# Performance work log

Measured on AMD Instinct MI355X. Metric: run time of the kernel, lower is better.

Reference implementation:

```python
import jax, jax.numpy as jnp
import numpy as np

N, E, H, NF, EF = 50000, 400000, 128, 10, 10


def setup_inputs() -> dict:
    key = jax.random.key(0)
    ks = iter(jax.random.split(key, 24))
    rn = lambda shape, s=0.1: jax.random.normal(next(ks), shape, jnp.float32) * s
    z = lambda shape: jnp.zeros(shape, jnp.float32)
    o = lambda shape: jnp.ones(shape, jnp.float32)
    return {
        "x": jax.random.normal(next(ks), (N, NF), jnp.float32),
        "edge_index": jax.random.randint(next(ks), (2, E), 0, N, jnp.int32),
        "edge_attr": jax.random.normal(next(ks), (E, EF), jnp.float32),
        "ne_w": rn((NF, H)), "ne_b": z(H), "ne_g": o(H), "ne_beta": z(H),
        "ee_w": rn((EF, H)), "ee_b": z(H), "ee_g": o(H), "ee_beta": z(H),
        "gate_w": rn((3 * H, H)), "gate_b": z(H),
        "gatA_w": rn((2, H, H)), "gatA_asrc": rn((2, 8, 16)), "gatA_adst": rn((2, 8, 16)), "gatA_bias": z((2, H)),
        "gatB_w": rn((H, H)), "gatB_asrc": rn((1, H)), "gatB_adst": rn((1, H)), "gatB_bias": z(H),
        "ln_g": o((3, H)), "ln_b": z((3, H)),
        "c1_w": rn((2 * H, H)), "c1_b": z(H), "cl1_g": o(H), "cl1_b": z(H),
        "c2_w": rn((H, H // 2)), "c2_b": z(H // 2), "cl2_g": o(H // 2), "cl2_b": z(H // 2),
        "c3_w": rn((H // 2, 2)), "c3_b": z(2),
    }


def _ln(x, g, b):
    m = x.mean(-1, keepdims=True)
    v = ((x - m) ** 2).mean(-1, keepdims=True)
    return (x - m) / jnp.sqrt(v + 1e-5) * g + b


def _gat(h, src, dst, n, w, asrc, adst, bias, concat):
    # PyG GATConv: lin (no bias), per-edge leaky_relu score, segment softmax over dst, scatter-add
    heads, dout = asrc.shape
    xp = (h @ w).reshape(n, heads, dout)             # [N, heads, dout]
    a_s = (xp * asrc).sum(-1)                        # [N, heads]
    a_d = (xp * adst).sum(-1)
    e = jax.nn.leaky_relu(a_s[src] + a_d[dst], 0.2)  # [E2, heads]
    m = jax.ops.segment_max(e, dst, num_segments=n)
    ex = jnp.exp(e - m[dst])
    s = jax.ops.segment_sum(ex, dst, num_segments=n)
    alpha = ex / s[dst]                               # [E2, heads]
    out = jax.ops.segment_sum(xp[src] * alpha[..., None], dst, num_segments=n)  # [N, heads, dout]
    out = out.reshape(n, heads * dout) if concat else out.mean(1)
    return out + bias


def reference(x, edge_index, edge_attr, ne_w, ne_b, ne_g, ne_beta, ee_w, ee_b, ee_g, ee_beta,
              gate_w, gate_b, gatA_w, gatA_asrc, gatA_adst, gatA_bias, gatB_w, gatB_asrc,
              gatB_adst, gatB_bias, ln_g, ln_b, c1_w, c1_b, cl1_g, cl1_b, c2_w, c2_b,
              cl2_g, cl2_b, c3_w, c3_b):
    n = x.shape[0]
    row, col = edge_index[0], edge_index[1]
    loops = jnp.arange(n, dtype=edge_index.dtype)     # GATConv add_self_loops=True
    src_sl = jnp.concatenate([row, loops])
    dst_sl = jnp.concatenate([col, loops])

    h = jax.nn.relu(_ln(x @ ne_w + ne_b, ne_g, ne_beta))      # node encoder (dropout=eval)
    for l in range(2):
        h = _gat(h, src_sl, dst_sl, n, gatA_w[l], gatA_asrc[l], gatA_adst[l], gatA_bias[l], True)
        h = jax.nn.relu(_ln(h, ln_g[l], ln_b[l]))
    h = _gat(h, src_sl, dst_sl, n, gatB_w, gatB_asrc, gatB_adst, gatB_bias, False)
    h = jax.nn.relu(_ln(h, ln_g[2], ln_b[2]))

    s = h[row]
    d = h[col]
    e = jax.nn.relu(_ln(edge_attr @ ee_w + ee_b, ee_g, ee_beta))  # edge encoder
    gate = jax.nn.sigmoid(jnp.concatenate([s, d, e], axis=1) @ gate_w + gate_b)
    s = s + gate * e
    d = d + gate * e

    zc = jax.nn.relu(_ln(jnp.concatenate([s, d], axis=1) @ c1_w + c1_b, cl1_g, cl1_b))
    zc = jax.nn.relu(_ln(zc @ c2_w + c2_b, cl2_g, cl2_b))
    return zc @ c3_w + c3_b                                   # [E, num_classes]
```

## Files before the change

### kernel.cpp

```cpp
#include <hip/hip_runtime.h>
#include <hip/hip_bf16.h>

#define H 128
#define NFEAT 10
#define EFEAT 10
#define XPS 144

typedef __attribute__((ext_vector_type(8))) short bf16x8;
typedef __attribute__((ext_vector_type(4))) float f32x4;
typedef __attribute__((ext_vector_type(16))) float f32x16;
typedef __attribute__((ext_vector_type(4))) unsigned u32x4;
typedef __attribute__((ext_vector_type(2))) unsigned u32x2;

__device__ __forceinline__ float bflo(unsigned v) { return __uint_as_float(v << 16); }
__device__ __forceinline__ float bfhi(unsigned v) { return __uint_as_float(v & 0xffff0000u); }
__device__ __forceinline__ unsigned bfpack(float a, float b) {
    __hip_bfloat16 h0 = __float2bfloat16(a), h1 = __float2bfloat16(b);
    return (unsigned)(*(unsigned short*)&h0) | ((unsigned)(*(unsigned short*)&h1) << 16);
}
__device__ __forceinline__ bf16x8 cast8(u32x4 v) { return __builtin_bit_cast(bf16x8, v); }

__device__ __forceinline__ bf16x8 frag_from_pack(const unsigned* w, int b2) {
    u32x4 t;
    t.x = w[b2 * 4 + 0];
    t.y = w[b2 * 4 + 1];
    t.z = w[b2 * 4 + 2];
    t.w = w[b2 * 4 + 3];
    return cast8(t);
}

template<int NT>
__device__ __forceinline__ void bias_ln_relu_pack(f32x16* acc, const float* __restrict__ bias,
        const float* __restrict__ g, const float* __restrict__ beta,
        int hh, float invn, unsigned (*pk)[8]) {
    float sm = 0.f;
#pragma unroll
    for (int m = 0; m < NT; m++) {
#pragma unroll
        for (int P = 0; P < 4; P++) {
            f32x4 bv = *(const f32x4*)&bias[m * 32 + P * 8 + hh * 4];
#pragma unroll
            for (int u = 0; u < 4; u++) {
                float v = acc[m][P * 4 + u] + bv[u];
                acc[m][P * 4 + u] = v;
                sm += v;
            }
        }
    }
    sm += __shfl_xor(sm, 32, 64);
    float mean = sm * invn;
    float q = 0.f;
#pragma unroll
    for (int m = 0; m < NT; m++) {
#pragma unroll
        for (int r = 0; r < 16; r++) { float d = acc[m][r] - mean; q += d * d; }
    }
    q += __shfl_xor(q, 32, 64);
    float rstd = rsqrtf(q * invn + 1e-5f);
#pragma unroll
    for (int m = 0; m < NT; m++) {
#pragma unroll
        for (int P = 0; P < 4; P++) {
            f32x4 gv = *(const f32x4*)&g[m * 32 + P * 8 + hh * 4];
            f32x4 bz = *(const f32x4*)&beta[m * 32 + P * 8 + hh * 4];
#pragma unroll
            for (int u = 0; u < 4; u++) {
                float y = fmaxf((acc[m][P * 4 + u] - mean) * rstd * gv[u] + bz[u], 0.f);
                acc[m][P * 4 + u] = y;
            }
        }
    }
#pragma unroll
    for (int m = 0; m < NT; m++) {
#pragma unroll
        for (int p = 0; p < 8; p++) pk[m][p] = bfpack(acc[m][2 * p], acc[m][2 * p + 1]);
    }
}

__global__ __launch_bounds__(256) void k_degree(const int* __restrict__ col,
                                                int* __restrict__ deg, int E, int N) {
    int i = blockIdx.x * blockDim.x + threadIdx.x;
    int E2 = E + N;
    if (i < E2) {
        int d = (i < E) ? col[i] : (i - E);
        atomicAdd(&deg[d], 1);
    }
}

__global__ __launch_bounds__(1024) void k_scan(const int* __restrict__ deg,
                                               int* __restrict__ offs,
                                               int* __restrict__ cursor, int N) {
    __shared__ int ps[1024];
    int t = threadIdx.x;
    int chunk = (N + 1023) / 1024;
    int begin = t * chunk;
    int end = begin + chunk; if (end > N) end = N;
    int s = 0;
    for (int i = begin; i < end; i++) s += deg[i];
    if (begin >= N) s = 0;
    ps[t] = s;
    __syncthreads();
    for (int off = 1; off < 1024; off <<= 1) {
        int v = (t >= off) ? ps[t - off] : 0;
        __syncthreads();
        ps[t] += v;
        __syncthreads();
    }
    int run = (t == 0) ? 0 : ps[t - 1];
    if (begin < N) {
        for (int i = begin; i < end; i++) {
            offs[i] = run;
            cursor[i] = run;
            run += deg[i];
        }
    }
    if (t == 1023) offs[N] = ps[1023];
}

__global__ __launch_bounds__(256) void k_scatter(const int* __restrict__ rowp,
                                                 const int* __restrict__ colp,
                                                 int* __restrict__ cursor,
                                                 int* __restrict__ srcs, int E, int N) {
    int i = blockIdx.x * blockDim.x + threadIdx.x;
    if (i < E + N) {
        int s, d;
        if (i < E) { s = rowp[i]; d = colp[i]; }
        else       { s = i - E;  d = i - E; }
        int pos = atomicAdd(&cursor[d], 1);
        srcs[pos] = s;
    }
}

__global__ __launch_bounds__(256) void k_node_enc(const float* __restrict__ x,
                                                  const float* __restrict__ wm,
                                                  const float* __restrict__ b,
                                                  const float* __restrict__ g,
                                                  const float* __restrict__ beta,
                                                  __hip_bfloat16* __restrict__ h, int N) {
    int t = threadIdx.x;
    int w = t >> 6, l = t & 63;
    int n = blockIdx.x * 4 + w;
    if (n >= N) return;
    float xs[NFEAT];
#pragma unroll
    for (int k = 0; k < NFEAT; k++) xs[k] = x[(size_t)n * NFEAT + k];
    float a0 = b[2 * l], a1 = b[2 * l + 1];
#pragma unroll
    for (int k = 0; k < NFEAT; k++) {
        float2 wv = *(const float2*)&wm[k * H + 2 * l];
        a0 += xs[k] * wv.x;
        a1 += xs[k] * wv.y;
    }
    float p = a0 + a1;
#pragma unroll
    for (int s = 1; s < 64; s <<= 1) p += __shfl_xor(p, s, 64);
    float mean = p * (1.0f / H);
    float d0 = a0 - mean, d1 = a1 - mean;
    float q = d0 * d0 + d1 * d1;
#pragma unroll
    for (int s = 1; s < 64; s <<= 1) q += __shfl_xor(q, s, 64);
    float rstd = rsqrtf(q * (1.0f / H) + 1e-5f);
    float y0 = fmaxf(d0 * rstd * g[2 * l] + beta[2 * l], 0.0f);
    float y1 = fmaxf(d1 * rstd * g[2 * l + 1] + beta[2 * l + 1], 0.0f);
    *(unsigned*)&h[(size_t)n * H + 2 * l] = bfpack(y0, y1);
}

__global__ __launch_bounds__(256, 2) void k_gat_xp_mfma(
        const __hip_bfloat16* __restrict__ h_bf,
        const __hip_bfloat16* __restrict__ wT,
        const float* __restrict__ asrc,
        const float* __restrict__ adst,
        __hip_bfloat16* __restrict__ xp_bf,
        float* __restrict__ a_d,
        int heads, int N) {
    __shared__ __hip_bfloat16 Ws[128 * 136];
    __shared__ __hip_bfloat16 As[64 * 136];
    int t = threadIdx.x;
    int n0 = blockIdx.x * 64;

#pragma unroll
    for (int it = 0; it < 2; it++) {
        int idx = it * 256 + t;
        int row = idx >> 2, seg = idx & 3;
        const uint4* src = (const uint4*)(wT + row * 128 + seg * 32);
        uint4 v0 = src[0], v1 = src[1], v2 = src[2], v3 = src[3];
        uint4* dst = (uint4*)&Ws[row * 136 + seg * 32];
        dst[0] = v0; dst[1] = v1; dst[2] = v2; dst[3] = v3;
    }
    {
        int row = t >> 2, seg = t & 3;
        int n = n0 + row; if (n >= N) n = N - 1;
        const uint4* src = (const uint4*)(h_bf + (size_t)n * 128 + seg * 32);
        uint4 v0 = src[0], v1 = src[1], v2 = src[2], v3 = src[3];
        uint4* dst = (uint4*)&As[row * 136 + seg * 32];
        dst[0] = v0; dst[1] = v1; dst[2] = v2; dst[3] = v3;
    }
    __syncthreads();

    int w = t >> 6, l = t & 63, ln15 = l & 15, quad = l >> 4, q8 = quad * 8;
    f32x4 acc[8] = {};
#pragma unroll
    for (int k = 0; k < 128; k += 32) {
        bf16x8 af = *(const bf16x8*)&As[(w * 16 + ln15) * 136 + k + q8];
#pragma unroll
        for (int i = 0; i < 8; i++) {
            bf16x8 bfr = *(const bf16x8*)&Ws[(i * 16 + ln15) * 136 + k + q8];
            acc[i] = __builtin_amdgcn_mfma_f32_16x16x32_bf16(af, bfr, acc[i], 0, 0, 0);
        }
    }

    if (heads == 8) {
#pragma unroll
        for (int i = 0; i < 8; i++) {
            float av = asrc[i * 16 + ln15], dvv = adst[i * 16 + ln15];
            float ps[4], pd[4];
#pragma unroll
            for (int r = 0; r < 4; r++) { ps[r] = acc[i][r] * av; pd[r] = acc[i][r] * dvv; }
#pragma unroll
            for (int s = 1; s < 16; s <<= 1) {
#pragma unroll
                for (int r = 0; r < 4; r++) {
                    ps[r] += __shfl_xor(ps[r], s, 64);
                    pd[r] += __shfl_xor(pd[r], s, 64);
                }
            }
            if (ln15 == 0) {
#pragma unroll
                for (int r = 0; r < 4; r++) {
                    int n = n0 + w * 16 + quad * 4 + r;
                    if (n < N) {
                        *(float*)&xp_bf[(size_t)n * XPS + 128 + 2 * i] = ps[r];
                        a_d[(size_t)n * 8 + i] = pd[r];
                    }
                }
            }
        }
    } else {
        float ps[4] = {0, 0, 0, 0}, pd[4] = {0, 0, 0, 0};
#pragma unroll
        for (int i = 0; i < 8; i++) {
            float av = asrc[i * 16 + ln15], dvv = adst[i * 16 + ln15];
#pragma unroll
            for (int r = 0; r < 4; r++) { ps[r] += acc[i][r] * av; pd[r] += acc[i][r] * dvv; }
        }
#pragma unroll
        for (int s = 1; s < 16; s <<= 1) {
#pragma unroll
            for (int r = 0; r < 4; r++) {
                ps[r] += __shfl_xor(ps[r], s, 64);
                pd[r] += __shfl_xor(pd[r], s, 64);
            }
        }
        if (ln15 == 0) {
#pragma unroll
            for (int r = 0; r < 4; r++) {
                int n = n0 + w * 16 + quad * 4 + r;
                if (n < N) {
                    *(float*)&xp_bf[(size_t)n * XPS + 128] = ps[r];
                    a_d[n] = pd[r];
                }
            }
        }
    }

#pragma unroll
    for (int i = 0; i < 8; i++) {
#pragma unroll
        for (int r = 0; r < 4; r++) {
            int n = n0 + w * 16 + quad * 4 + r;
            if (n < N) xp_bf[(size_t)n * XPS + i * 16 + ln15] = __float2bfloat16(acc[i][r]);
        }
    }
}

__global__ __launch_bounds__(256) void k_gat_agg(const __hip_bfloat16* __restrict__ xp,
                                                 const float* __restrict__ a_d,
                                                 const int* __restrict__ offs,
                                                 const int* __restrict__ srcs,
                                                 const float* __restrict__ bias,
                                                 const float* __restrict__ g,
                                                 const float* __restrict__ b,
                                                 __hip_bfloat16* __restrict__ hout,
                                                 int heads, int N) {
    int t = threadIdx.x;
    int w = t >> 6, l = t & 63;
    int n = blockIdx.x * 4 + w;
    if (n >= N) return;
    int head = (heads == 8) ? (l >> 3) : 0;
    float adv = a_d[(size_t)n * heads + head];
    int s0 = offs[n], s1 = offs[n + 1];
    float acc0 = 0.0f, acc1 = 0.0f, den = 0.0f;
    int j = s0;
    for (; j + 4 <= s1; j += 4) {
        int s_[4];
#pragma unroll
        for (int u = 0; u < 4; u++) s_[u] = srcs[j + u];
        float e_[4]; unsigned v_[4];
#pragma unroll
        for (int u = 0; u < 4; u++) {
            const __hip_bfloat16* xr = xp + (size_t)s_[u] * XPS;
            e_[u] = ((const float*)xr)[64 + head];
            v_[u] = *(const unsigned*)&xr[2 * l];
        }
#pragma unroll
        for (int u = 0; u < 4; u++) {
            float e = e_[u] + adv;
            e = (e >= 0.0f) ? e : 0.2f * e;
            float ex = __expf(e);
            den += ex;
            acc0 += ex * bflo(v_[u]);
            acc1 += ex * bfhi(v_[u]);
        }
    }
    for (; j < s1; j++) {
        int s = srcs[j];
        const __hip_bfloat16* xr = xp + (size_t)s * XPS;
        float e = ((const float*)xr)[64 + head] + adv;
        e = (e >= 0.0f) ? e : 0.2f * e;
        float ex = __expf(e);
        den += ex;
        unsigned v = *(const unsigned*)&xr[2 * l];
        acc0 += ex * bflo(v);
        acc1 += ex * bfhi(v);
    }
    float inv = 1.0f / den;
    float v0 = acc0 * inv + bias[2 * l];
    float v1 = acc1 * inv + bias[2 * l + 1];
    float p = v0 + v1;
#pragma unroll
    for (int s = 1; s < 64; s <<= 1) p += __shfl_xor(p, s, 64);
    float mean = p * (1.0f / H);
    float d0 = v0 - mean, d1 = v1 - mean;
    float q = d0 * d0 + d1 * d1;
#pragma unroll
    for (int s = 1; s < 64; s <<= 1) q += __shfl_xor(q, s, 64);
    float rstd = rsqrtf(q * (1.0f / H) + 1e-5f);
    float y0 = fmaxf(d0 * rstd * g[2 * l] + b[2 * l], 0.0f);
    float y1 = fmaxf(d1 * rstd * g[2 * l + 1] + b[2 * l + 1], 0.0f);
    *(unsigned*)&hout[(size_t)n * H + 2 * l] = bfpack(y0, y1);
}

__global__ __launch_bounds__(256) void k_wprep(const float* __restrict__ gate_w,
                                               const float* __restrict__ c1_w,
                                               const float* __restrict__ c2_w,
                                               const float* __restrict__ gatA_w,
                                               const float* __restrict__ gatB_w,
                                               const float* __restrict__ ee_w,
                                               __hip_bfloat16* __restrict__ gef_sw,
                                               __hip_bfloat16* __restrict__ c1s_sw,
                                               __hip_bfloat16* __restrict__ c2_sw,
                                               __hip_bfloat16* __restrict__ ee_sw,
                                               __hip_bfloat16* __restrict__ wT3,
                                               __hip_bfloat16* __restrict__ wpre4) {
    int i = blockIdx.x * blockDim.x + threadIdx.x;
    if (i < 16384) {
        int j = i & 7, l = (i >> 3) & 63, s = i >> 9;
        int m = s & 3, ks = s >> 2;
        int k = 256 + ks * 16 + 4 * (l >> 5) + (j & 3) + 8 * (j >> 2);
        int n = m * 32 + (l & 31);
        gef_sw[i] = __float2bfloat16(gate_w[k * 128 + n]);
    } else if (i < 32768) {
        int mm = i - 16384;
        int j = mm & 7, l = (mm >> 3) & 63, s = mm >> 9;
        int m = s & 3, ks = s >> 2;
        int k = ks * 16 + 4 * (l >> 5) + (j & 3) + 8 * (j >> 2);
        int n = m * 32 + (l & 31);
        c1s_sw[mm] = __float2bfloat16(c1_w[k * 128 + n] + c1_w[(128 + k) * 128 + n]);
    } else if (i < 40960) {
        int mm = i - 32768;
        int j = mm & 7, l = (mm >> 3) & 63, s = mm >> 9;
        int m = s & 1, ks = s >> 1;
        int k = ks * 16 + 4 * (l >> 5) + (j & 3) + 8 * (j >> 2);
        int n = m * 32 + (l & 31);
        c2_sw[mm] = __float2bfloat16(c2_w[k * 64 + n]);
    } else if (i < 43008) {
        int mm = i - 40960;
        int j = mm & 7, l = (mm >> 3) & 63, s = mm >> 9;
        int k = (l >> 5) * 8 + j;
        int n = s * 32 + (l & 31);
        ee_sw[mm] = (k < EFEAT) ? __float2bfloat16(ee_w[k * 128 + n]) : __float2bfloat16(0.0f);
    } else if (i < 92160) {
        int mm = i - 43008;
        int mat = mm / 16384, r = mm % 16384;
        int n = r / 128, k = r % 128;
        const float* src = (mat < 2) ? (gatA_w + (size_t)mat * 16384) : gatB_w;
        wT3[mm] = __float2bfloat16(src[k * 128 + n]);
    } else if (i < 157696) {
        int mm = i - 92160;
        int mat = mm / 16384, r = mm % 16384;
        int n = r / 128, k = r % 128;
        float v = (mat == 0) ? gate_w[k * 128 + n]
                : (mat == 1) ? gate_w[(128 + k) * 128 + n]
                : (mat == 2) ? c1_w[k * 128 + n]
                             : c1_w[(128 + k) * 128 + n];
        wpre4[mm] = __float2bfloat16(v);
    }
}

__global__ __launch_bounds__(256, 2) void k_pre_gemm(
        const __hip_bfloat16* __restrict__ h_bf,
        const __hip_bfloat16* __restrict__ wpre4,
        __hip_bfloat16* __restrict__ preS,
        __hip_bfloat16* __restrict__ preD, int N) {
    __shared__ __hip_bfloat16 Ws[128 * 136];
    __shared__ __hip_bfloat16 As[64 * 136];
    int t = threadIdx.x;
    int n0 = blockIdx.x * 64;
    int mat = blockIdx.y;
    const __hip_bfloat16* wT = wpre4 + (size_t)mat * 16384;

#pragma unroll
    for (int it = 0; it < 2; it++) {
        int idx = it * 256 + t;
        int row = idx >> 2, seg = idx & 3;
        const uint4* src = (const uint4*)(wT + row * 128 + seg * 32);
        uint4 v0 = src[0], v1 = src[1], v2 = src[2], v3 = src[3];
        uint4* dst = (uint4*)&Ws[row * 136 + seg * 32];
        dst[0] = v0; dst[1] = v1; dst[2] = v2; dst[3] = v3;
    }
    {
        int row = t >> 2, seg = t & 3;
        int n = n0 + row; if (n >= N) n = N - 1;
        const uint4* src = (const uint4*)(h_bf + (size_t)n * 128 + seg * 32);
        uint4 v0 = src[0], v1 = src[1], v2 = src[2], v3 = src[3];
        uint4* dst = (uint4*)&As[row * 136 + seg * 32];
        dst[0] = v0; dst[1] = v1; dst[2] = v2; dst[3] = v3;
    }
    __syncthreads();

    int w = t >> 6, l = t & 63, ln15 = l & 15, quad = l >> 4, q8 = quad * 8;
    f32x4 acc[8] = {};
#pragma unroll
    for (int k = 0; k < 128; k += 32) {
        bf16x8 af = *(const bf16x8*)&As[(w * 16 + ln15) * 136 + k + q8];
#pragma unroll
        for (int i = 0; i < 8; i++) {
            bf16x8 bfr = *(const bf16x8*)&Ws[(i * 16 + ln15) * 136 + k + q8];
            acc[i] = __builtin_amdgcn_mfma_f32_16x16x32_bf16(af, bfr, acc[i], 0, 0, 0);
        }
    }
    __hip_bfloat16* base = (mat & 1) ? preD : preS;
    int off = (mat >> 1) * 128;
#pragma unroll
    for (int i = 0; i < 8; i++) {
#pragma unroll
        for (int r = 0; r < 4; r++) {
            int n = n0 + w * 16 + quad * 4 + r;
            if (n < N) base[(size_t)n * 256 + off + i * 16 + ln15] = __float2bfloat16(acc[i][r]);
        }
    }
}

__global__ __launch_bounds__(256, 2) void k_edge_cls_v6(
        const int* __restrict__ rowp, const int* __restrict__ colp,
        const float* __restrict__ eattr,
        const __hip_bfloat16* __restrict__ preS,
        const __hip_bfloat16* __restrict__ preD,
        const __hip_bfloat16* __restrict__ ee_fa, const float* __restrict__ ee_b,
        const float* __restrict__ ee_g, const float* __restrict__ ee_beta,
        const __hip_bfloat16* __restrict__ gef_fa, const float* __restrict__ gate_b,
        const __hip_bfloat16* __restrict__ c1s_fa, const float* __restrict__ c1_b,
        const float* __restrict__ cl1_g, const float* __restrict__ cl1_b,
        const __hip_bfloat16* __restrict__ c2_fa, const float* __restrict__ c2_b,
        const float* __restrict__ cl2_g, const float* __restrict__ cl2_b,
        const float* __restrict__ c3_w, const float* __restrict__ c3_b,
        float* __restrict__ out, int E) {
    int t = threadIdx.x;
    int w = t >> 6, l = t & 63;
    int hh = l >> 5, e32 = l & 31;
    int eIdx = blockIdx.x * 128 + w * 32 + e32;
    int eF = (eIdx < E) ? eIdx : (E - 1);
    const unsigned short* pS = (const unsigned short*)preS + (size_t)rowp[eF] * 256;
    const unsigned short* pD = (const unsigned short*)preD + (size_t)colp[eF] * 256;

    unsigned efw[4][8];
    {
        const char* eb = (const char*)(eattr + (size_t)eF * EFEAT);
        float2 p0 = *(const float2*)(eb + (hh << 5));
        float2 p1 = *(const float2*)(eb + 8);
        float2 p2 = *(const float2*)(eb + 16);
        float2 p3 = *(const float2*)(eb + 24);
        if (hh) { p1.x = p1.y = 0.f; p2.x = p2.y = 0.f; p3.x = p3.y = 0.f; }
        u32x4 bwv;
        bwv.x = bfpack(p0.x, p0.y);
        bwv.y = bfpack(p1.x, p1.y);
        bwv.z = bfpack(p2.x, p2.y);
        bwv.w = bfpack(p3.x, p3.y);
        bf16x8 bb = cast8(bwv);
        f32x16 acc[4] = {};
#pragma unroll
        for (int m = 0; m < 4; m++) {
            bf16x8 a = *(const bf16x8*)(ee_fa + ((size_t)m * 64 + l) * 8);
            acc[m] = __builtin_amdgcn_mfma_f32_32x32x16_bf16(a, bb, acc[m], 0, 0, 0);
        }
        bias_ln_relu_pack<4>(acc, ee_b, ee_g, ee_beta, hh, 1.f / 128.f, efw);
    }

    f32x16 acc1[4] = {};
    {
        bf16x8 af[4];
#pragma unroll
        for (int s = 0; s < 4; s++) af[s] = *(const bf16x8*)(gef_fa + ((size_t)s * 64 + l) * 8);
#pragma unroll
        for (int ks = 0; ks < 8; ks++) {
            bf16x8 bb = frag_from_pack(efw[ks >> 1], ks & 1);
#pragma unroll
            for (int mt = 0; mt < 4; mt++) {
                int s = ks * 4 + mt;
                bf16x8 a = af[s & 3];
                if (s + 4 < 32) af[s & 3] = *(const bf16x8*)(gef_fa + ((size_t)(s + 4) * 64 + l) * 8);
                acc1[mt] = __builtin_amdgcn_mfma_f32_32x32x16_bf16(a, bb, acc1[mt], 0, 0, 0);
            }
        }
    }

    unsigned gew[4][8];
    {
#pragma unroll
        for (int m = 0; m < 4; m++) {
#pragma unroll
            for (int P = 0; P < 4; P++) {
                int f0 = m * 32 + P * 8 + hh * 4;
                f32x4 gb = *(const f32x4*)&gate_b[f0];
                u32x2 uw = *(const u32x2*)(pS + f0);
                u32x2 vw = *(const u32x2*)(pD + f0);
#pragma unroll
                for (int u2 = 0; u2 < 2; u2++) {
                    int p = P * 2 + u2;
                    unsigned uwd = u2 ? uw.y : uw.x;
                    unsigned vwd = u2 ? vw.y : vw.x;
                    float g0 = acc1[m][2 * p]     + bflo(uwd) + bflo(vwd) + gb[2 * u2];
                    float g1 = acc1[m][2 * p + 1] + bfhi(uwd) + bfhi(vwd) + gb[2 * u2 + 1];
                    g0 = 1.f / (1.f + __expf(-g0));
                    g1 = 1.f / (1.f + __expf(-g1));
                    gew[m][p] = bfpack(g0 * bflo(efw[m][p]), g1 * bfhi(efw[m][p]));
                }
            }
        }
    }

    unsigned z1w[4][8];
    {
        f32x16 acc2[4] = {};
        bf16x8 af[4];
#pragma unroll
        for (int s = 0; s < 4; s++) af[s] = *(const bf16x8*)(c1s_fa + ((size_t)s * 64 + l) * 8);
#pragma unroll
        for (int ks = 0; ks < 8; ks++) {
            bf16x8 bb = frag_from_pack(gew[ks >> 1], ks & 1);
#pragma unroll
            for (int mt = 0; mt < 4; mt++) {
                int s = ks * 4 + mt;
                bf16x8 a = af[s & 3];
                if (s + 4 < 32) af[s & 3] = *(const bf16x8*)(c1s_fa + ((size_t)(s + 4) * 64 + l) * 8);
                acc2[mt] = __builtin_amdgcn_mfma_f32_32x32x16_bf16(a, bb, acc2[mt], 0, 0, 0);
            }
        }
#pragma unroll
        for (int m = 0; m < 4; m++) {
#pragma unroll
            for (int P = 0; P < 4; P++) {
                int f0 = m * 32 + P * 8 + hh * 4;
                u32x2 pw = *(const u32x2*)(pS + 128 + f0);
                u32x2 qw = *(const u32x2*)(pD + 128 + f0);
                acc2[m][P * 4 + 0] += bflo(pw.x) + bflo(qw.x);
                acc2[m][P * 4 + 1] += bfhi(pw.x) + bfhi(qw.x);
                acc2[m][P * 4 + 2] += bflo(pw.y) + bflo(qw.y);
                acc2[m][P * 4 + 3] += bfhi(pw.y) + bfhi(qw.y);
            }
        }
        bias_ln_relu_pack<4>(acc2, c1_b, cl1_g, cl1_b, hh, 1.f / 128.f, z1w);
    }

    {
        f32x16 acc3[2] = {};
        bf16x8 af[4];
#pragma unroll
        for (int s = 0; s < 4; s++) af[s] = *(const bf16x8*)(c2_fa + ((size_t)s * 64 + l) * 8);
#pragma unroll
        for (int ks = 0; ks < 8; ks++) {
            bf16x8 bb = frag_from_pack(z1w[ks >> 1], ks & 1);
#pragma unroll
            for (int mt = 0; mt < 2; mt++) {
                int s = ks * 2 + mt;
                bf16x8 a = af[s & 3];
                if (s + 4 < 16) af[s & 3] = *(const bf16x8*)(c2_fa + ((size_t)(s + 4) * 64 + l) * 8);
                acc3[mt] = __builtin_amdgcn_mfma_f32_32x32x16_bf16(a, bb, acc3[mt], 0, 0, 0);
            }
        }
        float sm = 0.f;
#pragma unroll
        for (int m = 0; m < 2; m++) {
#pragma unroll
            for (int P = 0; P < 4; P++) {
                f32x4 bv = *(const f32x4*)&c2_b[m * 32 + P * 8 + hh * 4];
#pragma unroll
                for (int u = 0; u < 4; u++) {
                    float v = acc3[m][P * 4 + u] + bv[u];
                    acc3[m][P * 4 + u] = v;
                    sm += v;
                }
            }
        }
        sm += __shfl_xor(sm, 32, 64);
        float mean = sm * (1.f / 64.f);
        float q = 0.f;
#pragma unroll
        for (int m = 0; m < 2; m++) {
#pragma unroll
            for (int r = 0; r < 16; r++) { float d = acc3[m][r] - mean; q += d * d; }
        }
        q += __shfl_xor(q, 32, 64);
        float rstd = rsqrtf(q * (1.f / 64.f) + 1e-5f);
        float s0 = 0.f, s1 = 0.f;
#pragma unroll
        for (int m = 0; m < 2; m++) {
#pragma unroll
            for (int P = 0; P < 4; P++) {
                int f0 = m * 32 + P * 8 + hh * 4;
                f32x4 gv = *(const f32x4*)&cl2_g[f0];
                f32x4 bz = *(const f32x4*)&cl2_b[f0];
                f32x4 wA = *(const f32x4*)&c3_w[f0 * 2];
                f32x4 wB = *(const f32x4*)&c3_w[f0 * 2 + 4];
#pragma unroll
                for (int u = 0; u < 4; u++) {
                    float y = fmaxf((acc3[m][P * 4 + u] - mean) * rstd * gv[u] + bz[u], 0.f);
                    float wc0 = (u < 2) ? wA[2 * u] : wB[2 * u - 4];
                    float wc1 = (u < 2) ? wA[2 * u + 1] : wB[2 * u - 3];
                    s0 += y * wc0;
                    s1 += y * wc1;
                }
            }
        }
        s0 += __shfl_xor(s0, 32, 64);
        s1 += __shfl_xor(s1, 32, 64);
        if (hh == 0 && eIdx < E) {
            float2 o; o.x = s0 + c3_b[0]; o.y = s1 + c3_b[1];
            *(float2*)&out[(size_t)eIdx * 2] = o;
        }
    }
}

extern "C" void kernel_launch(void* const* d_in, const int* in_sizes, int n_in,
                              void* d_out, int out_size, void* d_ws, size_t ws_size,
                              hipStream_t stream) {
    const float* x        = (const float*)d_in[0];
    const int*   eidx     = (const int*)d_in[1];
    const float* eattr    = (const float*)d_in[2];
    const float* ne_w     = (const float*)d_in[3];
    const float* ne_b     = (const float*)d_in[4];
    const float* ne_g     = (const float*)d_in[5];
    const float* ne_beta  = (const float*)d_in[6];
    const float* ee_w     = (const float*)d_in[7];
    const float* ee_b     = (const float*)d_in[8];
    const float* ee_g     = (const float*)d_in[9];
    const float* ee_beta  = (const float*)d_in[10];
    const float* gate_w   = (const float*)d_in[11];
    const float* gate_b   = (const float*)d_in[12];
    const float* gatA_w   = (const float*)d_in[13];
    const float* gatA_as  = (const float*)d_in[14];
    const float* gatA_ad  = (const float*)d_in[15];
    const float* gatA_bias= (const float*)d_in[16];
    const float* gatB_w   = (const float*)d_in[17];
    const float* gatB_as  = (const float*)d_in[18];
    const float* gatB_ad  = (const float*)d_in[19];
    const float* gatB_bias= (const float*)d_in[20];
    const float* ln_g     = (const float*)d_in[21];
    const float* ln_b     = (const float*)d_in[22];
    const float* c1_w     = (const float*)d_in[23];
    const float* c1_b     = (const float*)d_in[24];
    const float* cl1_g    = (const float*)d_in[25];
    const float* cl1_b    = (const float*)d_in[26];
    const float* c2_w     = (const float*)d_in[27];
    const float* c2_b     = (const float*)d_in[28];
    const float* cl2_g    = (const float*)d_in[29];
    const float* cl2_b    = (const float*)d_in[30];
    const float* c3_w     = (const float*)d_in[31];
    const float* c3_b     = (const float*)d_in[32];

    const int N = in_sizes[0] / NFEAT;
    const int E = in_sizes[1] / 2;
    const int E2 = E + N;
    const int* rowp = eidx;
    const int* colp = eidx + E;

    char* ws = (char*)d_ws;
    size_t off = 0;
    auto alloc = [&](size_t bytes) -> void* {
        void* p = ws + off;
        off = (off + bytes + 255) & ~(size_t)255;
        return p;
    };
    int*   deg    = (int*)alloc((size_t)N * 4);
    int*   cursor = (int*)alloc((size_t)N * 4);
    int*   offs   = (int*)alloc((size_t)(N + 1) * 4);
    int*   srcs   = (int*)alloc((size_t)E2 * 4);
    float* a_d    = (float*)alloc((size_t)N * 8 * 4);
    __hip_bfloat16* h_bfA  = (__hip_bfloat16*)alloc((size_t)N * H * 2);
    __hip_bfloat16* h_bfB  = (__hip_bfloat16*)alloc((size_t)N * H * 2);
    __hip_bfloat16* xp_bf  = (__hip_bfloat16*)alloc((size_t)N * XPS * 2);
    __hip_bfloat16* gef_sw = (__hip_bfloat16*)alloc((size_t)16384 * 2);
    __hip_bfloat16* c1s_sw = (__hip_bfloat16*)alloc((size_t)16384 * 2);
    __hip_bfloat16* c2_sw  = (__hip_bfloat16*)alloc((size_t)8192 * 2);
    __hip_bfloat16* ee_sw  = (__hip_bfloat16*)alloc((size_t)2048 * 2);
    __hip_bfloat16* wT3    = (__hip_bfloat16*)alloc((size_t)3 * 128 * 128 * 2);
    __hip_bfloat16* wpre4  = (__hip_bfloat16*)alloc((size_t)4 * 128 * 128 * 2);
    __hip_bfloat16* preS   = (__hip_bfloat16*)alloc((size_t)N * 256 * 2);
    __hip_bfloat16* preD   = (__hip_bfloat16*)alloc((size_t)N * 256 * 2);
    (void)ws_size;

    k_wprep<<<(157696 + 255) / 256, 256, 0, stream>>>(gate_w, c1_w, c2_w, gatA_w, gatB_w, ee_w,
                                                      gef_sw, c1s_sw, c2_sw, ee_sw, wT3, wpre4);

    hipMemsetAsync(deg, 0, (size_t)N * 4, stream);
    k_degree<<<(E2 + 255) / 256, 256, 0, stream>>>(colp, deg, E, N);
    k_scan<<<1, 1024, 0, stream>>>(deg, offs, cursor, N);
    k_scatter<<<(E2 + 255) / 256, 256, 0, stream>>>(rowp, colp, cursor, srcs, E, N);

    int ngrid = (N + 3) / 4;
    k_node_enc<<<ngrid, 256, 0, stream>>>(x, ne_w, ne_b, ne_g, ne_beta, h_bfA, N);

    int xpgrid = (N + 63) / 64;
    __hip_bfloat16* hin = h_bfA;
    __hip_bfloat16* hout = h_bfB;
    for (int l = 0; l < 2; l++) {
        k_gat_xp_mfma<<<xpgrid, 256, 0, stream>>>(hin, wT3 + (size_t)l * 16384,
                                                  gatA_as + l * H, gatA_ad + l * H,
                                                  xp_bf, a_d, 8, N);
        k_gat_agg<<<ngrid, 256, 0, stream>>>(xp_bf, a_d, offs, srcs,
                                             gatA_bias + l * H, ln_g + l * H, ln_b + l * H,
                                             hout, 8, N);
        __hip_bfloat16* tmp = hin; hin = hout; hout = tmp;
    }
    k_gat_xp_mfma<<<xpgrid, 256, 0, stream>>>(hin, wT3 + (size_t)2 * 16384,
                                              gatB_as, gatB_ad,
                                              xp_bf, a_d, 1, N);
    k_gat_agg<<<ngrid, 256, 0, stream>>>(xp_bf, a_d, offs, srcs,
                                         gatB_bias, ln_g + 2 * H, ln_b + 2 * H,
                                         hout, 1, N);

    dim3 gpre(xpgrid, 4);
    k_pre_gemm<<<gpre, 256, 0, stream>>>(hout, wpre4, preS, preD, N);

    k_edge_cls_v6<<<(E + 127) / 128, 256, 0, stream>>>(
        rowp, colp, eattr, preS, preD,
        ee_sw, ee_b, ee_g, ee_beta,
        gef_sw, gate_b,
        c1s_sw, c1_b, cl1_g, cl1_b,
        c2_sw, c2_b, cl2_g, cl2_b,
        c3_w, c3_b,
        (float*)d_out, E);
}
```

Baseline: 691.0 us.

## Stage edge activations through LDS instead of registers to raise occupancy

The fused edge classifier used to hold the encoded edge features, gated features and first-layer outputs as packed bf16 registers. It now writes each activation row to a per-wave LDS buffer and reads MFMA B fragments back from LDS. The weight swizzle k-ordering is changed so the fragments are contiguous 8-element slices, and the register-prefetch ring for A fragments is dropped. Fewer live registers allow launch bounds of 3 blocks per CU. The cost is LDS traffic, fewer prefetched weight loads, and a non-unrolled k loop.

```diff
diff --git a/kernel.cpp b/kernel.cpp
--- a/kernel.cpp
+++ b/kernel.cpp
@@ -5,6 +5,7 @@
 #define NFEAT 10
 #define EFEAT 10
 #define XPS 144
+#define BROW 136
 
 typedef __attribute__((ext_vector_type(8))) short bf16x8;
 typedef __attribute__((ext_vector_type(4))) float f32x4;
@@ -20,19 +21,10 @@
 }
 __device__ __forceinline__ bf16x8 cast8(u32x4 v) { return __builtin_bit_cast(bf16x8, v); }
 
-__device__ __forceinline__ bf16x8 frag_from_pack(const unsigned* w, int b2) {
-    u32x4 t;
-    t.x = w[b2 * 4 + 0];
-    t.y = w[b2 * 4 + 1];
-    t.z = w[b2 * 4 + 2];
-    t.w = w[b2 * 4 + 3];
-    return cast8(t);
-}
-
 template<int NT>
-__device__ __forceinline__ void bias_ln_relu_pack(f32x16* acc, const float* __restrict__ bias,
+__device__ __forceinline__ void bias_ln_relu_st(f32x16* acc, const float* __restrict__ bias,
         const float* __restrict__ g, const float* __restrict__ beta,
-        int hh, float invn, unsigned (*pk)[8]) {
+        int hh, float invn, __hip_bfloat16* Brow) {
     float sm = 0.f;
 #pragma unroll
     for (int m = 0; m < NT; m++) {
@@ -73,7 +65,10 @@
 #pragma unroll
     for (int m = 0; m < NT; m++) {
 #pragma unroll
-        for (int p = 0; p < 8; p++) pk[m][p] = bfpack(acc[m][2 * p], acc[m][2 * p + 1]);
+        for (int p = 0; p < 8; p++) {
+            int feat = 32 * m + 8 * (p >> 1) + 4 * hh + 2 * (p & 1);
+            *(unsigned*)&Brow[feat] = bfpack(acc[m][2 * p], acc[m][2 * p + 1]);
+        }
     }
 }
 
@@ -356,21 +351,21 @@
     if (i < 16384) {
         int j = i & 7, l = (i >> 3) & 63, s = i >> 9;
         int m = s & 3, ks = s >> 2;
-        int k = 256 + ks * 16 + 4 * (l >> 5) + (j & 3) + 8 * (j >> 2);
+        int k = 256 + ks * 16 + 8 * (l >> 5) + j;
         int n = m * 32 + (l & 31);
         gef_sw[i] = __float2bfloat16(gate_w[k * 128 + n]);
     } else if (i < 32768) {
         int mm = i - 16384;
         int j = mm & 7, l = (mm >> 3) & 63, s = mm >> 9;
         int m = s & 3, ks = s >> 2;
-        int k = ks * 16 + 4 * (l >> 5) + (j & 3) + 8 * (j >> 2);
+        int k = ks * 16 + 8 * (l >> 5) + j;
         int n = m * 32 + (l & 31);
         c1s_sw[mm] = __float2bfloat16(c1_w[k * 128 + n] + c1_w[(128 + k) * 128 + n]);
     } else if (i < 40960) {
         int mm = i - 32768;
         int j = mm & 7, l = (mm >> 3) & 63, s = mm >> 9;
         int m = s & 1, ks = s >> 1;
-        int k = ks * 16 + 4 * (l >> 5) + (j & 3) + 8 * (j >> 2);
+        int k = ks * 16 + 8 * (l >> 5) + j;
         int n = m * 32 + (l & 31);
         c2_sw[mm] = __float2bfloat16(c2_w[k * 64 + n]);
     } else if (i < 43008) {
@@ -451,7 +446,7 @@
     }
 }
 
-__global__ __launch_bounds__(256, 2) void k_edge_cls_v6(
+__global__ __launch_bounds__(256, 3) void k_edge_cls_v7(
         const int* __restrict__ rowp, const int* __restrict__ colp,
         const float* __restrict__ eattr,
         const __hip_bfloat16* __restrict__ preS,
@@ -465,15 +460,17 @@
         const float* __restrict__ cl2_g, const float* __restrict__ cl2_b,
         const float* __restrict__ c3_w, const float* __restrict__ c3_b,
         float* __restrict__ out, int E) {
+    __shared__ __hip_bfloat16 Bs[4 * 32 * BROW];
     int t = threadIdx.x;
     int w = t >> 6, l = t & 63;
     int hh = l >> 5, e32 = l & 31;
+    __hip_bfloat16* B = Bs + w * (32 * BROW);
+    __hip_bfloat16* Brow = B + e32 * BROW;
     int eIdx = blockIdx.x * 128 + w * 32 + e32;
     int eF = (eIdx < E) ? eIdx : (E - 1);
     const unsigned short* pS = (const unsigned short*)preS + (size_t)rowp[eF] * 256;
     const unsigned short* pD = (const unsigned short*)preD + (size_t)colp[eF] * 256;
 
-    unsigned efw[4][8];
     {
         const char* eb = (const char*)(eattr + (size_t)eF * EFEAT);
         float2 p0 = *(const float2*)(eb + (hh << 5));
@@ -493,28 +490,21 @@
             bf16x8 a = *(const bf16x8*)(ee_fa + ((size_t)m * 64 + l) * 8);
             acc[m] = __builtin_amdgcn_mfma_f32_32x32x16_bf16(a, bb, acc[m], 0, 0, 0);
         }
-        bias_ln_relu_pack<4>(acc, ee_b, ee_g, ee_beta, hh, 1.f / 128.f, efw);
+        bias_ln_relu_st<4>(acc, ee_b, ee_g, ee_beta, hh, 1.f / 128.f, Brow);
     }
 
     f32x16 acc1[4] = {};
     {
-        bf16x8 af[4];
-#pragma unroll
-        for (int s = 0; s < 4; s++) af[s] = *(const bf16x8*)(gef_fa + ((size_t)s * 64 + l) * 8);
-#pragma unroll
+        const bf16x8* wp = (const bf16x8*)gef_fa + l;
         for (int ks = 0; ks < 8; ks++) {
-            bf16x8 bb = frag_from_pack(efw[ks >> 1], ks & 1);
-#pragma unroll
-            for (int mt = 0; mt < 4; mt++) {
-                int s = ks * 4 + mt;
-                bf16x8 a = af[s & 3];
-                if (s + 4 < 32) af[s & 3] = *(const bf16x8*)(gef_fa + ((size_t)(s + 4) * 64 + l) * 8);
-                acc1[mt] = __builtin_amdgcn_mfma_f32_32x32x16_bf16(a, bb, acc1[mt], 0, 0, 0);
-            }
-        }
-    }
-
-    unsigned gew[4][8];
+            bf16x8 bb = *(const bf16x8*)&B[e32 * BROW + ks * 16 + hh * 8];
+#pragma unroll
+            for (int mt = 0; mt < 4; mt++)
+                acc1[mt] = __builtin_amdgcn_mfma_f32_32x32x16_bf16(
+                    wp[(size_t)(ks * 4 + mt) * 64], bb, acc1[mt], 0, 0, 0);
+        }
+    }
+
     {
 #pragma unroll
         for (int m = 0; m < 4; m++) {
@@ -533,28 +523,22 @@
                     float g1 = acc1[m][2 * p + 1] + bfhi(uwd) + bfhi(vwd) + gb[2 * u2 + 1];
                     g0 = 1.f / (1.f + __expf(-g0));
                     g1 = 1.f / (1.f + __expf(-g1));
-                    gew[m][p] = bfpack(g0 * bflo(efw[m][p]), g1 * bfhi(efw[m][p]));
+                    unsigned ew = *(unsigned*)&Brow[f0 + 2 * u2];
+                    *(unsigned*)&Brow[f0 + 2 * u2] = bfpack(g0 * bflo(ew), g1 * bfhi(ew));
                 }
             }
         }
     }
 
-    unsigned z1w[4][8];
     {
         f32x16 acc2[4] = {};
-        bf16x8 af[4];
-#pragma unroll
-        for (int s = 0; s < 4; s++) af[s] = *(const bf16x8*)(c1s_fa + ((size_t)s * 64 + l) * 8);
-#pragma unroll
+        const bf16x8* wp = (const bf16x8*)c1s_fa + l;
         for (int ks = 0; ks < 8; ks++) {
-            bf16x8 bb = frag_from_pack(gew[ks >> 1], ks & 1);
-#pragma unroll
-            for (int mt = 0; mt < 4; mt++) {
-                int s = ks * 4 + mt;
-                bf16x8 a = af[s & 3];
-                if (s + 4 < 32) af[s & 3] = *(const bf16x8*)(c1s_fa + ((size_t)(s + 4) * 64 + l) * 8);
-                acc2[mt] = __builtin_amdgcn_mfma_f32_32x32x16_bf16(a, bb, acc2[mt], 0, 0, 0);
-            }
+            bf16x8 bb = *(const bf16x8*)&B[e32 * BROW + ks * 16 + hh * 8];
+#pragma unroll
+            for (int mt = 0; mt < 4; mt++)
+                acc2[mt] = __builtin_amdgcn_mfma_f32_32x32x16_bf16(
+                    wp[(size_t)(ks * 4 + mt) * 64], bb, acc2[mt], 0, 0, 0);
         }
 #pragma unroll
         for (int m = 0; m < 4; m++) {
@@ -569,24 +553,18 @@
                 acc2[m][P * 4 + 3] += bfhi(pw.y) + bfhi(qw.y);
             }
         }
-        bias_ln_relu_pack<4>(acc2, c1_b, cl1_g, cl1_b, hh, 1.f / 128.f, z1w);
+        bias_ln_relu_st<4>(acc2, c1_b, cl1_g, cl1_b, hh, 1.f / 128.f, Brow);
     }
 
     {
         f32x16 acc3[2] = {};
-        bf16x8 af[4];
-#pragma unroll
-        for (int s = 0; s < 4; s++) af[s] = *(const bf16x8*)(c2_fa + ((size_t)s * 64 + l) * 8);
-#pragma unroll
+        const bf16x8* wp = (const bf16x8*)c2_fa + l;
         for (int ks = 0; ks < 8; ks++) {
-            bf16x8 bb = frag_from_pack(z1w[ks >> 1], ks & 1);
-#pragma unroll
-            for (int mt = 0; mt < 2; mt++) {
-                int s = ks * 2 + mt;
-                bf16x8 a = af[s & 3];
-                if (s + 4 < 16) af[s & 3] = *(const bf16x8*)(c2_fa + ((size_t)(s + 4) * 64 + l) * 8);
-                acc3[mt] = __builtin_amdgcn_mfma_f32_32x32x16_bf16(a, bb, acc3[mt], 0, 0, 0);
-            }
+            bf16x8 bb = *(const bf16x8*)&B[e32 * BROW + ks * 16 + hh * 8];
+#pragma unroll
+            for (int mt = 0; mt < 2; mt++)
+                acc3[mt] = __builtin_amdgcn_mfma_f32_32x32x16_bf16(
+                    wp[(size_t)(ks * 2 + mt) * 64], bb, acc3[mt], 0, 0, 0);
         }
         float sm = 0.f;
 #pragma unroll
@@ -742,7 +720,7 @@
     dim3 gpre(xpgrid, 4);
     k_pre_gemm<<<gpre, 256, 0, stream>>>(hout, wpre4, preS, preD, N);
 
-    k_edge_cls_v6<<<(E + 127) / 128, 256, 0, stream>>>(
+    k_edge_cls_v7<<<(E + 127) / 128, 256, 0, stream>>>(
         rowp, colp, eattr, preS, preD,
         ee_sw, ee_b, ee_g, ee_beta,
         gef_sw, gate_b,
```

New measurement: 718.2 us. 1.04x slower.
